# Kernel optimization log

Measured on AMD Instinct MI355X. Metric: run time of the kernel, lower is better.

## Reference

```python
import jax, jax.numpy as jnp
import numpy as np

D_MODEL = 1024
D_FF = 4096
N_EXPERTS = 8
TOP_K = 2

def setup_inputs() -> dict:
    key = jax.random.key(0)
    ks = jax.random.split(key, 6)
    s = lambda fan_in: 1.0 / np.sqrt(fan_in)
    x = jax.random.normal(ks[0], (4, 2048, D_MODEL), dtype=jnp.float32)
    Wg = jax.random.normal(ks[1], (D_MODEL, N_EXPERTS), dtype=jnp.float32) * s(D_MODEL)
    W1 = jax.random.normal(ks[2], (N_EXPERTS, D_MODEL, D_FF), dtype=jnp.float32) * s(D_MODEL)
    b1 = jax.random.normal(ks[3], (N_EXPERTS, D_FF), dtype=jnp.float32) * 0.01
    W2 = jax.random.normal(ks[4], (N_EXPERTS, D_FF, D_MODEL), dtype=jnp.float32) * s(D_FF)
    b2 = jax.random.normal(ks[5], (N_EXPERTS, D_MODEL), dtype=jnp.float32) * 0.01
    return {"x": x, "Wg": Wg, "W1": W1, "b1": b1, "W2": W2, "b2": b2}

def reference(x, Wg, W1, b1, W2, b2):
    B, L, D = x.shape
    xf = x.reshape(B * L, D)               # (N, D)
    N = xf.shape[0]
    E = Wg.shape[1]
    # gating
    logits = xf @ Wg                        # (N, E)
    probs = jax.nn.softmax(logits, axis=-1)
    topv, topi = jax.lax.top_k(probs, TOP_K)          # (N, K)
    w = topv / (topv.sum(axis=-1, keepdims=True) + 1e-9)
    rows = jnp.arange(N)[:, None]
    combine = jnp.zeros((N, E), xf.dtype).at[rows, topi].set(w)    # (N, E) combine weights
    dispatch = jnp.zeros((N, E), xf.dtype).at[rows, topi].set(1.0)
    aux_loss = (dispatch.mean(axis=0) * probs.mean(axis=0)).sum() * E
    # experts: dense per-expert FFN, masked-combined (zero weight => zero contribution),
    # mathematically identical to the torch masked gather/scatter loop.
    out = jnp.zeros_like(xf)
    for e in range(E):  # fixed small loop over experts
        h = jax.nn.gelu(xf @ W1[e] + b1[e], approximate=False)   # (N, d_ff)
        out = out + combine[:, e:e + 1] * (h @ W2[e] + b2[e])
    return out.reshape(B, L, D), aux_loss
```

## Files before the change

### kernel.cpp

```cpp
#include <hip/hip_runtime.h>
#include <math.h>

#define D_MODEL 1024
#define D_FF    4096
#define NEXP    8
#define NTOK    8192
#define NASSIGN (NTOK*2)
#define NGBLK   (NTOK/4)

using short8 = __attribute__((ext_vector_type(8))) short;
using short4v = __attribute__((ext_vector_type(4))) short;
using f32x4  = __attribute__((ext_vector_type(4))) float;

__device__ __forceinline__ short f2bf(float f) {
  unsigned u = __float_as_uint(f);
  unsigned r = (u + 0x7fffu + ((u >> 16) & 1u)) >> 16;
  return (short)r;
}
__device__ __forceinline__ float bf2f(unsigned short u) {
  return __uint_as_float(((unsigned)u) << 16);
}

__device__ __forceinline__ void gload_lds16(const void* g, void* l) {
  __builtin_amdgcn_global_load_lds((const __attribute__((address_space(1))) void*)g,
                                   (__attribute__((address_space(3))) void*)l, 16, 0, 0);
}

__device__ __forceinline__ float gelu_f(float x) {
  float z = 0.70710678118f * x;
  float a = fabsf(z);
  float t = 1.0f / (1.0f + 0.3275911f * a);
  float p = t * (0.254829592f + t * (-0.284496736f + t * (1.421413741f +
            t * (-1.453152027f + t * 1.061405429f))));
  float er = 1.0f - p * __expf(-a * a);
  er = copysignf(er, z);
  return 0.5f * x * (1.0f + er);
}

__global__ void zero_kernel(int* ctrl) {
  int i = threadIdx.x;
  if (i < 24) ctrl[i] = 0;
}

__global__ __launch_bounds__(256) void transpose_conv(const float* __restrict__ in, short* __restrict__ out,
                                                      int R, int C) {
  __shared__ float t[64][65];
  int e = blockIdx.z;
  size_t base = (size_t)e * R * C;
  int r0 = blockIdx.y * 64, c0 = blockIdx.x * 64;
  int lr = threadIdx.x >> 6, lc = threadIdx.x & 63;
#pragma unroll
  for (int j = 0; j < 16; ++j) {
    int rr = lr + j * 4;
    t[rr][lc] = in[base + (size_t)(r0 + rr) * C + c0 + lc];
  }
  __syncthreads();
  int tid = threadIdx.x;
#pragma unroll
  for (int p = 0; p < 2; ++p) {
    int oc = p * 32 + (tid >> 3);
    int rseg = (tid & 7) * 8;
    short8 v;
#pragma unroll
    for (int q = 0; q < 8; ++q) v[q] = f2bf(t[rseg + q][oc]);
    *(short8*)&out[base + (size_t)(c0 + oc) * R + r0 + rseg] = v;
  }
}

__global__ __launch_bounds__(256) void gating_kernel(const float* __restrict__ x, const float* __restrict__ Wg,
                                                     int* __restrict__ assign_e, float* __restrict__ assign_w,
                                                     int* __restrict__ cnt_part, float* __restrict__ psum_part,
                                                     ushort4* __restrict__ xb4) {
  __shared__ float l_ps[NEXP];
  __shared__ int   l_cnt[NEXP];
  int tid = threadIdx.x, wv = tid >> 6, lane = tid & 63;
  if (tid < NEXP) { l_ps[tid] = 0.f; l_cnt[tid] = 0; }
  __syncthreads();

  int t = blockIdx.x * 4 + wv;
  const float4* xr = (const float4*)(x + (size_t)t * D_MODEL);
  float acc[NEXP];
#pragma unroll
  for (int e = 0; e < NEXP; ++e) acc[e] = 0.f;
#pragma unroll
  for (int i = 0; i < 4; ++i) {
    int c4 = lane + 64 * i;
    float4 v = xr[c4];
    ushort4 o;
    o.x = (unsigned short)f2bf(v.x); o.y = (unsigned short)f2bf(v.y);
    o.z = (unsigned short)f2bf(v.z); o.w = (unsigned short)f2bf(v.w);
    xb4[(size_t)t * 256 + c4] = o;
    const float* wr = Wg + c4 * 4 * NEXP;
#pragma unroll
    for (int j = 0; j < 4; ++j) {
      float xv = (&v.x)[j];
#pragma unroll
      for (int e = 0; e < NEXP; ++e) acc[e] += xv * wr[j * NEXP + e];
    }
  }
#pragma unroll
  for (int off = 32; off; off >>= 1)
#pragma unroll
    for (int e = 0; e < NEXP; ++e) acc[e] += __shfl_down(acc[e], off);

  if (lane == 0) {
    float m = acc[0];
#pragma unroll
    for (int e = 1; e < NEXP; ++e) m = fmaxf(m, acc[e]);
    float p[NEXP], s = 0.f;
#pragma unroll
    for (int e = 0; e < NEXP; ++e) { p[e] = expf(acc[e] - m); s += p[e]; }
    float inv = 1.f / s;
#pragma unroll
    for (int e = 0; e < NEXP; ++e) p[e] *= inv;
    int i0 = 0; float v0 = p[0];
#pragma unroll
    for (int e = 1; e < NEXP; ++e) if (p[e] > v0) { v0 = p[e]; i0 = e; }
    int i1 = -1; float v1 = -1.f;
#pragma unroll
    for (int e = 0; e < NEXP; ++e) if (e != i0 && p[e] > v1) { v1 = p[e]; i1 = e; }
    float denom = 1.f / (v0 + v1 + 1e-9f);
    assign_e[2 * t] = i0;     assign_w[2 * t] = v0 * denom;
    assign_e[2 * t + 1] = i1; assign_w[2 * t + 1] = v1 * denom;
    atomicAdd(&l_cnt[i0], 1);
    atomicAdd(&l_cnt[i1], 1);
#pragma unroll
    for (int e = 0; e < NEXP; ++e) atomicAdd(&l_ps[e], p[e]);
  }
  __syncthreads();
  if (tid < NEXP) {
    psum_part[blockIdx.x * NEXP + tid] = l_ps[tid];
    cnt_part[blockIdx.x * NEXP + tid] = l_cnt[tid];
  }
}

__global__ __launch_bounds__(256) void scan_kernel(const int* __restrict__ cnt_part, const float* __restrict__ psum_part,
                                                   int* __restrict__ cnt, int* __restrict__ offs,
                                                   float* __restrict__ aux_out) {
  __shared__ float sp[256];
  __shared__ int   sc[256];
  int tid = threadIdx.x;
  int e = tid & 7, c = tid >> 3;
  float fs = 0.f; int is = 0;
  for (int b = c; b < NGBLK; b += 32) {
    fs += psum_part[b * NEXP + e];
    is += cnt_part[b * NEXP + e];
  }
  sp[tid] = fs; sc[tid] = is;
  __syncthreads();
  if (tid < NEXP) {
    float f = 0.f; int n = 0;
    for (int c2 = 0; c2 < 32; ++c2) { f += sp[c2 * 8 + tid]; n += sc[c2 * 8 + tid]; }
    cnt[tid] = n; sp[tid] = f;
  }
  __syncthreads();
  if (tid == 0) {
    int o = 0; float aux = 0.f;
    for (int e2 = 0; e2 < NEXP; ++e2) {
      offs[e2] = o; o += cnt[e2];
      aux += (float)cnt[e2] * sp[e2];
    }
    aux_out[0] = aux * (float)NEXP / ((float)NTOK * (float)NTOK);
  }
}

__global__ __launch_bounds__(256) void scatter_kernel(const int* __restrict__ assign_e,
                                                      const int* __restrict__ offs, int* __restrict__ cursor,
                                                      int* __restrict__ slot_tok, int* __restrict__ slot_of) {
  __shared__ int lhist[NEXP], lbase[NEXP];
  int tid = threadIdx.x;
  int a = blockIdx.x * 256 + tid;
  if (tid < NEXP) lhist[tid] = 0;
  __syncthreads();
  int e = assign_e[a];
  int lp = atomicAdd(&lhist[e], 1);
  __syncthreads();
  if (tid < NEXP) lbase[tid] = atomicAdd(&cursor[tid], lhist[tid]);
  __syncthreads();
  int s = offs[e] + lbase[e] + lp;
  slot_tok[s] = a >> 1;
  slot_of[a] = s;
}

template<int KD, int ND, int RT, int EPI, bool RTOUT>
__global__ __launch_bounds__(512, 2) void gemm8p(
    const short* __restrict__ Asrc, const short* __restrict__ Bsrc,
    const float* __restrict__ bias, const int* __restrict__ slot_tok,
    const int* __restrict__ cnt, const int* __restrict__ offs,
    short* __restrict__ OutP)
{
  constexpr int NT = KD / 64;
  constexpr int NP = ND / 256;
  constexpr int NPAN = NEXP * NP / 8;
  extern __shared__ char ldsb[];

  int bid = blockIdx.x;
  int x = bid & 7, j = bid >> 3;
  int k, rt;
  if (RTOUT) { rt = j / NPAN; k = j - rt * NPAN; }
  else       { k = j / RT;    rt = j - k * RT; }
  int ft = k % NP;
  int e = (x + k) & 7;
  int cn = cnt[e];
  if (rt * 256 >= cn) return;
  int off = offs[e];
  int tid = threadIdx.x, l = tid & 63, w = tid >> 6;
  int wm = w >> 2, wn = w & 3;
  int l15 = l & 15, kh = l >> 4;

  int srw = tid >> 3;
  int swz = ((tid & 7) ^ (srw & 7)) * 8;
  const short* ar[4];
  const short* br[4];
#pragma unroll
  for (int s = 0; s < 4; ++s) {
    int gr = rt * 256 + s * 64 + srw;
    int ic = gr < cn ? gr : cn - 1;
    if (EPI == 0) ar[s] = Asrc + (size_t)slot_tok[off + ic] * KD + swz;
    else          ar[s] = Asrc + (size_t)(off + ic) * KD + swz;
    br[s] = Bsrc + (size_t)e * ND * KD + (size_t)(ft * 256 + s * 64 + srw) * KD + swz;
  }

#define STAGE(P, TAU) do {                                                        \
    int _b = (TAU) & 1;                                                           \
    const short* _p0 = ((P) >= 2 ? ar : br)[(P) & 1];                             \
    const short* _p1 = ((P) >= 2 ? ar : br)[((P) & 1) + 2];                       \
    char* _d = ldsb + _b * 65536 + ((P) >= 2 ? 0 : 32768);                        \
    gload_lds16(_p0 + (size_t)(TAU) * 64, _d + ((P) & 1) * 8192 + tid * 16);      \
    gload_lds16(_p1 + (size_t)(TAU) * 64, _d + (((P) & 1) + 2) * 8192 + tid * 16);\
  } while (0)

  STAGE(0, 0); STAGE(1, 0); STAGE(2, 0); STAGE(3, 0);
  STAGE(0, 1); STAGE(1, 1); STAGE(2, 1);
  asm volatile("s_waitcnt vmcnt(6)" ::: "memory");
  asm volatile("s_barrier" ::: "memory");

  int cx0 = ((0 * 4 + kh) ^ (l15 & 7)) << 4;
  int cx1 = ((1 * 4 + kh) ^ (l15 & 7)) << 4;
  int arow = (wm * 128 + l15) << 7;
  int brow = (wn * 64 + l15) << 7;
  f32x4 acc[8][4] = {};
  short8 bq0[4], bq1[4], afA[4], afB[4];

  for (int t = 0; t < NT; ++t) {
    const char* Ab = ldsb + (t & 1) * 65536;
    const char* Bb = Ab + 32768;
#pragma unroll
    for (int n = 0; n < 4; ++n) bq0[n] = *(const short8*)(Bb + brow + (n << 11) + cx0);
#pragma unroll
    for (int n = 0; n < 4; ++n) bq1[n] = *(const short8*)(Bb + brow + (n << 11) + cx1);
#pragma unroll
    for (int m = 0; m < 4; ++m) afA[m] = *(const short8*)(Ab + arow + ((m * 16) << 7) + cx0);
    if (t + 1 < NT) STAGE(3, t + 1);
#pragma unroll
    for (int m = 0; m < 4; ++m) afB[m] = *(const short8*)(Ab + arow + ((64 + m * 16) << 7) + cx0);
    asm volatile("s_barrier" ::: "memory");
    __builtin_amdgcn_s_setprio(1);
#pragma unroll
    for (int m = 0; m < 4; ++m)
#pragma unroll
      for (int n = 0; n < 4; ++n)
        acc[m][n] = __builtin_amdgcn_mfma_f32_16x16x32_bf16(bq0[n], afA[m], acc[m][n], 0, 0, 0);
    __builtin_amdgcn_s_setprio(0);
    asm volatile("s_barrier" ::: "memory");
    if (t + 2 < NT) STAGE(0, t + 2);
#pragma unroll
    for (int m = 0; m < 4; ++m) afA[m] = *(const short8*)(Ab + arow + ((m * 16) << 7) + cx1);
    asm volatile("s_barrier" ::: "memory");
    __builtin_amdgcn_s_setprio(1);
#pragma unroll
    for (int m = 0; m < 4; ++m)
#pragma unroll
      for (int n = 0; n < 4; ++n)
        acc[4 + m][n] = __builtin_amdgcn_mfma_f32_16x16x32_bf16(bq0[n], afB[m], acc[4 + m][n], 0, 0, 0);
    __builtin_amdgcn_s_setprio(0);
    asm volatile("s_barrier" ::: "memory");
    if (t + 2 < NT) STAGE(1, t + 2);
#pragma unroll
    for (int m = 0; m < 4; ++m) afB[m] = *(const short8*)(Ab + arow + ((64 + m * 16) << 7) + cx1);
    asm volatile("s_barrier" ::: "memory");
    __builtin_amdgcn_s_setprio(1);
#pragma unroll
    for (int m = 0; m < 4; ++m)
#pragma unroll
      for (int n = 0; n < 4; ++n)
        acc[m][n] = __builtin_amdgcn_mfma_f32_16x16x32_bf16(bq1[n], afA[m], acc[m][n], 0, 0, 0);
    __builtin_amdgcn_s_setprio(0);
    asm volatile("s_barrier" ::: "memory");
    if (t + 2 < NT) STAGE(2, t + 2);
    asm volatile("s_barrier" ::: "memory");
    __builtin_amdgcn_s_setprio(1);
#pragma unroll
    for (int m = 0; m < 4; ++m)
#pragma unroll
      for (int n = 0; n < 4; ++n)
        acc[4 + m][n] = __builtin_amdgcn_mfma_f32_16x16x32_bf16(bq1[n], afB[m], acc[4 + m][n], 0, 0, 0);
    __builtin_amdgcn_s_setprio(0);
    if (t < NT - 2)       { asm volatile("s_waitcnt vmcnt(6)" ::: "memory"); }
    else if (t == NT - 2) { asm volatile("s_waitcnt vmcnt(0)" ::: "memory"); }
    asm volatile("s_barrier" ::: "memory");
  }
#undef STAGE

  int ftb = ft * 256;
  f32x4 b4[4];
#pragma unroll
  for (int n = 0; n < 4; ++n) b4[n] = *(const f32x4*)&bias[e * ND + ftb + wn * 64 + n * 16 + kh * 4];

  char* slab = ldsb + w * 2048;
#pragma unroll
  for (int mi = 0; mi < 8; ++mi) {
#pragma unroll
    for (int n = 0; n < 4; ++n) {
      short4v h;
#pragma unroll
      for (int jj = 0; jj < 4; ++jj) {
        float v = acc[mi][n][jj] + b4[n][jj];
        if (EPI == 0) v = gelu_f(v);
        h[jj] = f2bf(v);
      }
      int chunk = n * 2 + (kh >> 1);
      *(short4v*)(slab + l15 * 128 + ((chunk ^ (l15 & 7)) << 4) + ((kh & 1) << 3)) = h;
    }
    int tr = l >> 2;
    int tok = rt * 256 + wm * 128 + mi * 16 + tr;
    if (tok < cn) {
#pragma unroll
      for (int cc = 0; cc < 2; ++cc) {
        int c2 = (l & 3) * 2 + cc;
        short8 v = *(const short8*)(slab + tr * 128 + ((c2 ^ (tr & 7)) << 4));
        *(short8*)&OutP[(size_t)(off + tok) * ND + ftb + wn * 64 + c2 * 8] = v;
      }
    }
    asm volatile("s_waitcnt lgkmcnt(0)" ::: "memory");
  }
}

__global__ __launch_bounds__(256) void combine_kernel(const unsigned short* __restrict__ y,
                                                      const int* __restrict__ slot_of,
                                                      const float* __restrict__ assign_w, float* __restrict__ out) {
  int t = blockIdx.x;
  int d4 = threadIdx.x;
  int s0 = slot_of[2 * t], s1 = slot_of[2 * t + 1];
  float w0 = assign_w[2 * t], w1 = assign_w[2 * t + 1];
  ushort4 a = ((const ushort4*)(y + (size_t)s0 * D_MODEL))[d4];
  ushort4 b = ((const ushort4*)(y + (size_t)s1 * D_MODEL))[d4];
  float4 o;
  o.x = w0 * bf2f(a.x) + w1 * bf2f(b.x);
  o.y = w0 * bf2f(a.y) + w1 * bf2f(b.y);
  o.z = w0 * bf2f(a.z) + w1 * bf2f(b.z);
  o.w = w0 * bf2f(a.w) + w1 * bf2f(b.w);
  ((float4*)(out + (size_t)t * D_MODEL))[d4] = o;
}

extern "C" void kernel_launch(void* const* d_in, const int* in_sizes, int n_in,
                              void* d_out, int out_size, void* d_ws, size_t ws_size,
                              hipStream_t stream) {
  const float* x  = (const float*)d_in[0];
  const float* Wg = (const float*)d_in[1];
  const float* W1 = (const float*)d_in[2];
  const float* b1 = (const float*)d_in[3];
  const float* W2 = (const float*)d_in[4];
  const float* b2 = (const float*)d_in[5];
  float* out = (float*)d_out;
  char* ws = (char*)d_ws;

  short* xb       = (short*)(ws);
  short* w1t      = (short*)(ws + 16777216);
  short* y        = (short*)(ws + 16777216);
  short* w2t      = (short*)(ws + 83886080);
  short* H        = (short*)(ws + 150994944);
  int*   slot_tok = (int*)  (ws + 285212672);
  int*   assign_e = (int*)  (ws + 285278208);
  float* assign_w = (float*)(ws + 285343744);
  int*   slot_of  = (int*)  (ws + 285409280);
  int*   cnt_part = (int*)  (ws + 285474816);
  float* psum_part= (float*)(ws + 285540352);
  int*   ctrl     = (int*)  (ws + 285605888);
  int* cnt = ctrl; int* cursor = ctrl + 8; int* offs = ctrl + 16;

  hipFuncSetAttribute(reinterpret_cast<const void*>(&gemm8p<D_MODEL, D_FF, 12, 0, false>),
                      hipFuncAttributeMaxDynamicSharedMemorySize, 131072);
  hipFuncSetAttribute(reinterpret_cast<const void*>(&gemm8p<D_FF, D_MODEL, 12, 1, true>),
                      hipFuncAttributeMaxDynamicSharedMemorySize, 131072);

  zero_kernel<<<1, 64, 0, stream>>>(ctrl);
  transpose_conv<<<dim3(64, 16, NEXP), 256, 0, stream>>>(W1, w1t, D_MODEL, D_FF);
  transpose_conv<<<dim3(16, 64, NEXP), 256, 0, stream>>>(W2, w2t, D_FF, D_MODEL);
  gating_kernel<<<NGBLK, 256, 0, stream>>>(x, Wg, assign_e, assign_w, cnt_part, psum_part,
                                           (ushort4*)xb);
  scan_kernel<<<1, 256, 0, stream>>>(cnt_part, psum_part, cnt, offs, out + (out_size - 1));
  scatter_kernel<<<NASSIGN / 256, 256, 0, stream>>>(assign_e, offs, cursor, slot_tok, slot_of);
  gemm8p<D_MODEL, D_FF, 12, 0, false><<<8 * 16 * 12, 512, 131072, stream>>>(
      xb, w1t, b1, slot_tok, cnt, offs, H);
  gemm8p<D_FF, D_MODEL, 12, 1, true><<<8 * 4 * 12, 512, 131072, stream>>>(
      H, w2t, b2, slot_tok, cnt, offs, y);
  combine_kernel<<<NTOK, 256, 0, stream>>>((const unsigned short*)y, slot_of, assign_w, out);
}
```

Measured before the change: 554.9 us.

## Restructure expert GEMM pipeline with upfront fragment loads and fewer barriers

The GEMM main loop now reads all four A fragment groups and both B groups from LDS at the start of each k-step. It then issues the next-stage global-to-LDS copies in two grouped bursts, cutting the barriers per iteration roughly in half. Stage pointers are advanced incrementally instead of recomputed, and the vmcnt waits are tightened. Separately, the zero_kernel launch is removed and the cursor reset is folded into scan_kernel. The costs are higher register pressure from the extra fragment arrays, and a possible race: the next B tile is written into the same LDS buffer before the barrier that guarantees every wave has finished reading it.

```diff
diff --git a/kernel.cpp b/kernel.cpp
--- a/kernel.cpp
+++ b/kernel.cpp
@@ -37,11 +37,6 @@
   return 0.5f * x * (1.0f + er);
 }
 
-__global__ void zero_kernel(int* ctrl) {
-  int i = threadIdx.x;
-  if (i < 24) ctrl[i] = 0;
-}
-
 __global__ __launch_bounds__(256) void transpose_conv(const float* __restrict__ in, short* __restrict__ out,
                                                       int R, int C) {
   __shared__ float t[64][65];
@@ -136,7 +131,7 @@
 
 __global__ __launch_bounds__(256) void scan_kernel(const int* __restrict__ cnt_part, const float* __restrict__ psum_part,
                                                    int* __restrict__ cnt, int* __restrict__ offs,
-                                                   float* __restrict__ aux_out) {
+                                                   int* __restrict__ cursor, float* __restrict__ aux_out) {
   __shared__ float sp[256];
   __shared__ int   sc[256];
   int tid = threadIdx.x;
@@ -152,6 +147,7 @@
     float f = 0.f; int n = 0;
     for (int c2 = 0; c2 < 32; ++c2) { f += sp[c2 * 8 + tid]; n += sc[c2 * 8 + tid]; }
     cnt[tid] = n; sp[tid] = f;
+    cursor[tid] = 0;
   }
   __syncthreads();
   if (tid == 0) {
@@ -220,19 +216,23 @@
     else          ar[s] = Asrc + (size_t)(off + ic) * KD + swz;
     br[s] = Bsrc + (size_t)e * ND * KD + (size_t)(ft * 256 + s * 64 + srw) * KD + swz;
   }
-
-#define STAGE(P, TAU) do {                                                        \
-    int _b = (TAU) & 1;                                                           \
-    const short* _p0 = ((P) >= 2 ? ar : br)[(P) & 1];                             \
-    const short* _p1 = ((P) >= 2 ? ar : br)[((P) & 1) + 2];                       \
-    char* _d = ldsb + _b * 65536 + ((P) >= 2 ? 0 : 32768);                        \
-    gload_lds16(_p0 + (size_t)(TAU) * 64, _d + ((P) & 1) * 8192 + tid * 16);      \
-    gload_lds16(_p1 + (size_t)(TAU) * 64, _d + (((P) & 1) + 2) * 8192 + tid * 16);\
+  const short* p0a = br[0]; const short* p0b = br[2];
+  const short* p1a = br[1]; const short* p1b = br[3];
+  const short* p2a = ar[0]; const short* p2b = ar[2];
+  const short* p3a = ar[1]; const short* p3b = ar[3];
+
+#define STAGEP(P, BUFBIT) do {                                                   \
+    char* _d = ldsb + (BUFBIT) * 65536 + ((P) >= 2 ? 0 : 32768)                  \
+             + ((P) & 1) * 8192 + tid * 16;                                      \
+    gload_lds16(p##P##a, _d); gload_lds16(p##P##b, _d + 16384);                  \
+    p##P##a += 64; p##P##b += 64;                                                \
   } while (0)
-
-  STAGE(0, 0); STAGE(1, 0); STAGE(2, 0); STAGE(3, 0);
-  STAGE(0, 1); STAGE(1, 1); STAGE(2, 1);
-  asm volatile("s_waitcnt vmcnt(6)" ::: "memory");
+#define STG(P, B) do { if (P == 0) STAGEP(0, B); else if (P == 1) STAGEP(1, B);  \
+                       else if (P == 2) STAGEP(2, B); else STAGEP(3, B); } while (0)
+
+  STAGEP(0, 0); STAGEP(1, 0); STAGEP(2, 0); STAGEP(3, 0);
+  STAGEP(0, 1); STAGEP(1, 1); STAGEP(2, 1);
+  asm volatile("s_waitcnt vmcnt(3)" ::: "memory");
   asm volatile("s_barrier" ::: "memory");
 
   int cx0 = ((0 * 4 + kh) ^ (l15 & 7)) << 4;
@@ -240,7 +240,7 @@
   int arow = (wm * 128 + l15) << 7;
   int brow = (wn * 64 + l15) << 7;
   f32x4 acc[8][4] = {};
-  short8 bq0[4], bq1[4], afA[4], afB[4];
+  short8 bq0[4], bq1[4], afA[4], afB[4], afC[4], afD[4];
 
   for (int t = 0; t < NT; ++t) {
     const char* Ab = ldsb + (t & 1) * 65536;
@@ -251,9 +251,14 @@
     for (int n = 0; n < 4; ++n) bq1[n] = *(const short8*)(Bb + brow + (n << 11) + cx1);
 #pragma unroll
     for (int m = 0; m < 4; ++m) afA[m] = *(const short8*)(Ab + arow + ((m * 16) << 7) + cx0);
-    if (t + 1 < NT) STAGE(3, t + 1);
 #pragma unroll
     for (int m = 0; m < 4; ++m) afB[m] = *(const short8*)(Ab + arow + ((64 + m * 16) << 7) + cx0);
+#pragma unroll
+    for (int m = 0; m < 4; ++m) afC[m] = *(const short8*)(Ab + arow + ((m * 16) << 7) + cx1);
+#pragma unroll
+    for (int m = 0; m < 4; ++m) afD[m] = *(const short8*)(Ab + arow + ((64 + m * 16) << 7) + cx1);
+    if (t + 1 < NT) STG(3, (t + 1) & 1);
+    if (t + 2 < NT) STG(0, t & 1);
     asm volatile("s_barrier" ::: "memory");
     __builtin_amdgcn_s_setprio(1);
 #pragma unroll
@@ -261,13 +266,6 @@
 #pragma unroll
       for (int n = 0; n < 4; ++n)
         acc[m][n] = __builtin_amdgcn_mfma_f32_16x16x32_bf16(bq0[n], afA[m], acc[m][n], 0, 0, 0);
-    __builtin_amdgcn_s_setprio(0);
-    asm volatile("s_barrier" ::: "memory");
-    if (t + 2 < NT) STAGE(0, t + 2);
-#pragma unroll
-    for (int m = 0; m < 4; ++m) afA[m] = *(const short8*)(Ab + arow + ((m * 16) << 7) + cx1);
-    asm volatile("s_barrier" ::: "memory");
-    __builtin_amdgcn_s_setprio(1);
 #pragma unroll
     for (int m = 0; m < 4; ++m)
 #pragma unroll
@@ -275,32 +273,26 @@
         acc[4 + m][n] = __builtin_amdgcn_mfma_f32_16x16x32_bf16(bq0[n], afB[m], acc[4 + m][n], 0, 0, 0);
     __builtin_amdgcn_s_setprio(0);
     asm volatile("s_barrier" ::: "memory");
-    if (t + 2 < NT) STAGE(1, t + 2);
-#pragma unroll
-    for (int m = 0; m < 4; ++m) afB[m] = *(const short8*)(Ab + arow + ((64 + m * 16) << 7) + cx1);
+    if (t + 2 < NT) { STG(1, t & 1); STG(2, t & 1); }
     asm volatile("s_barrier" ::: "memory");
     __builtin_amdgcn_s_setprio(1);
 #pragma unroll
     for (int m = 0; m < 4; ++m)
 #pragma unroll
       for (int n = 0; n < 4; ++n)
-        acc[m][n] = __builtin_amdgcn_mfma_f32_16x16x32_bf16(bq1[n], afA[m], acc[m][n], 0, 0, 0);
+        acc[m][n] = __builtin_amdgcn_mfma_f32_16x16x32_bf16(bq1[n], afC[m], acc[m][n], 0, 0, 0);
+#pragma unroll
+    for (int m = 0; m < 4; ++m)
+#pragma unroll
+      for (int n = 0; n < 4; ++n)
+        acc[4 + m][n] = __builtin_amdgcn_mfma_f32_16x16x32_bf16(bq1[n], afD[m], acc[4 + m][n], 0, 0, 0);
     __builtin_amdgcn_s_setprio(0);
-    asm volatile("s_barrier" ::: "memory");
-    if (t + 2 < NT) STAGE(2, t + 2);
-    asm volatile("s_barrier" ::: "memory");
-    __builtin_amdgcn_s_setprio(1);
-#pragma unroll
-    for (int m = 0; m < 4; ++m)
-#pragma unroll
-      for (int n = 0; n < 4; ++n)
-        acc[4 + m][n] = __builtin_amdgcn_mfma_f32_16x16x32_bf16(bq1[n], afB[m], acc[4 + m][n], 0, 0, 0);
-    __builtin_amdgcn_s_setprio(0);
-    if (t < NT - 2)       { asm volatile("s_waitcnt vmcnt(6)" ::: "memory"); }
+    if (t < NT - 2)       { asm volatile("s_waitcnt vmcnt(3)" ::: "memory"); }
     else if (t == NT - 2) { asm volatile("s_waitcnt vmcnt(0)" ::: "memory"); }
     asm volatile("s_barrier" ::: "memory");
   }
-#undef STAGE
+#undef STG
+#undef STAGEP
 
   int ftb = ft * 256;
   f32x4 b4[4];
@@ -384,12 +376,11 @@
   hipFuncSetAttribute(reinterpret_cast<const void*>(&gemm8p<D_FF, D_MODEL, 12, 1, true>),
                       hipFuncAttributeMaxDynamicSharedMemorySize, 131072);
 
-  zero_kernel<<<1, 64, 0, stream>>>(ctrl);
   transpose_conv<<<dim3(64, 16, NEXP), 256, 0, stream>>>(W1, w1t, D_MODEL, D_FF);
   transpose_conv<<<dim3(16, 64, NEXP), 256, 0, stream>>>(W2, w2t, D_FF, D_MODEL);
   gating_kernel<<<NGBLK, 256, 0, stream>>>(x, Wg, assign_e, assign_w, cnt_part, psum_part,
                                            (ushort4*)xb);
-  scan_kernel<<<1, 256, 0, stream>>>(cnt_part, psum_part, cnt, offs, out + (out_size - 1));
+  scan_kernel<<<1, 256, 0, stream>>>(cnt_part, psum_part, cnt, offs, cursor, out + (out_size - 1));
   scatter_kernel<<<NASSIGN / 256, 256, 0, stream>>>(assign_e, offs, cursor, slot_tok, slot_of);
   gemm8p<D_MODEL, D_FF, 12, 0, false><<<8 * 16 * 12, 512, 131072, stream>>>(
       xb, w1t, b1, slot_tok, cnt, offs, H);
```

After: 579.5 us. +4.4%, slower.
